# Kernel optimization log

Hardware: AMD Instinct MI355X
Metric: run time of the kernel (lower is better)

The kernel has to match this reference:

```python
import jax, jax.numpy as jnp
import numpy as np

B, S, D = 8, 2048, 128

def setup_inputs() -> dict:
    key = jax.random.key(0)
    kq, kk, kv, km = jax.random.split(key, 4)
    q = jax.random.normal(kq, (B, S, D), dtype=jnp.float32)
    k = jax.random.normal(kk, (B, S, D), dtype=jnp.float32)
    v = jax.random.normal(kv, (B, S, D), dtype=jnp.float32)
    mask = jax.random.randint(km, (B, S), 0, 2).astype(bool)  # True = masked out
    return {"q": q, "k": k, "v": v, "mask": mask}

def reference(q, k, v, mask):
    scaler = np.sqrt(D).astype(np.float32)
    # score[b, i, j] = <q_i, k_j> / sqrt(d_k)
    score = jnp.einsum('bik,bjk->bij', q, k) / scaler
    score = score - jnp.max(score, axis=-1, keepdims=True)
    e = jnp.exp(score)
    # mask is (B, S_kv): broadcast across query positions, zero out masked keys
    e = jnp.where(mask[:, None, :], 0.0, e)
    a = e / jnp.sum(e, axis=-1, keepdims=True)
    c = jnp.einsum('bij,bjd->bid', a, v)
    return c
```

## Files before the change

kernel.cpp:

```cpp
#include <hip/hip_runtime.h>
#include <hip/hip_fp16.h>
#include <math.h>

typedef __attribute__((ext_vector_type(8))) short short8;
typedef __attribute__((ext_vector_type(16))) float floatx16;
typedef __attribute__((ext_vector_type(2))) __bf16 bf16x2;
typedef __attribute__((ext_vector_type(2))) unsigned int uint2v;

namespace {
constexpr int Bn = 8;
constexpr int Sn = 2048;
constexpr int Dn = 128;
constexpr int BQ = 128;
constexpr int BK = 64;
constexpr int QTILES = Sn / BQ;
constexpr int NKB = Sn / BK;
constexpr int ROWS = Bn * Sn;
constexpr int NSPLIT = 4;
constexpr float SC2 = 0.12753102063642597f;
constexpr float DEFER_THR = 8.0f;
constexpr int TILE_USH = BK * Dn;
}

#if __has_builtin(__builtin_amdgcn_exp2f)
#define EXP2(x) __builtin_amdgcn_exp2f(x)
#else
#define EXP2(x) exp2f(x)
#endif

__device__ __forceinline__ unsigned short f2bf(float x) {
  union { float f; unsigned u; } a; a.f = x;
  unsigned r = a.u + 0x7fffu + ((a.u >> 16) & 1u);
  return (unsigned short)(r >> 16);
}

__device__ __forceinline__ unsigned pack2bf(float x, float y) {
  union { bf16x2 b; unsigned u; } c;
  c.b[0] = (__bf16)x; c.b[1] = (__bf16)y;
  return c.u;
}

__device__ __forceinline__ uint2v pl32swap(unsigned a, unsigned b, int h) {
#if __has_builtin(__builtin_amdgcn_permlane32_swap)
  (void)h;
  return __builtin_amdgcn_permlane32_swap(a, b, false, false);
#else
  unsigned ax = __shfl_xor((int)a, 32);
  unsigned bx = __shfl_xor((int)b, 32);
  uint2v r;
  r[0] = h ? bx : a;
  r[1] = h ? b : ax;
  return r;
#endif
}

__device__ __forceinline__ void gl_lds16(const void* g, void* l, int lane) {
#if __has_builtin(__builtin_amdgcn_global_load_lds)
  (void)lane;
  __builtin_amdgcn_global_load_lds((const __attribute__((address_space(1))) unsigned int*)g,
                                   (__attribute__((address_space(3))) unsigned int*)l, 16, 0, 0);
#else
  *(float4*)((char*)l + lane * 16) = *(const float4*)g;
#endif
}

__global__ __launch_bounds__(256)
void prep(const float* __restrict__ kg, const float* __restrict__ vg,
          const unsigned char* __restrict__ mraw,
          unsigned short* __restrict__ Kpg, unsigned short* __restrict__ Vpg,
          float* __restrict__ mb2g) {
  __shared__ __align__(16) float Vf[16 * 136];
  const int p = blockIdx.x;
  const int b = p >> 7, q = p & 127;
  const int kb = q >> 2, k16 = q & 3;
  const int t = threadIdx.x;

  unsigned wv = ((const unsigned int*)mraw)[t];
  int any1  = __syncthreads_or((wv & 0x0000ff00u) ? 1 : 0);
  int any23 = __syncthreads_or((wv & 0xffff0000u) ? 1 : 0);
  const int mlayout = any1 ? 1 : (any23 ? 2 : 0);
  if (p < 64) {
    int idx = p * 256 + t;
    bool ms;
    if (mlayout == 1)      ms = mraw[idx] != 0;
    else if (mlayout == 2) ms = ((const float*)mraw)[idx] != 0.0f;
    else                   ms = ((const int*)mraw)[idx] != 0;
    mb2g[idx] = ms ? -1e30f : 0.0f;
  }

  const int j  = t >> 4;
  const int o8 = t & 15;
  const size_t base = ((size_t)(b * Sn + kb * 64 + k16 * 16 + j)) * 32 + o8 * 2;
  const float4* k4 = (const float4*)kg;
  const float4* v4 = (const float4*)vg;

  {
    float4 a = k4[base], bq = k4[base + 1];
    union { unsigned u[4]; short8 s8; } pk;
    pk.u[0] = pack2bf(a.x, a.y);   pk.u[1] = pack2bf(a.z, a.w);
    pk.u[2] = pack2bf(bq.x, bq.y); pk.u[3] = pack2bf(bq.z, bq.w);
    const int jl = k16 * 16 + j;
    *(short8*)(Kpg + (size_t)(b * NKB + kb) * TILE_USH + jl * 128 + ((o8 ^ (jl & 7)) * 8)) = pk.s8;
  }
  {
    float4 a = v4[base], bq = v4[base + 1];
    *(float4*)&Vf[j * 136 + o8 * 8]     = a;
    *(float4*)&Vf[j * 136 + o8 * 8 + 4] = bq;
  }
  __syncthreads();
  {
    const int d = t >> 1, h = t & 1;
    union { unsigned u[4]; short8 s8; } pv;
    #pragma unroll
    for (int i = 0; i < 4; ++i)
      pv.u[i] = pack2bf(Vf[(h * 8 + 2 * i) * 136 + d], Vf[(h * 8 + 2 * i + 1) * 136 + d]);
    const int og = k16 * 2 + h;
    *(short8*)(Vpg + (size_t)(b * NKB + kb) * TILE_USH + d * 64 + ((og ^ (d & 7)) * 8)) = pv.s8;
  }
}


__device__ __forceinline__ void stage_tile(const char* gsrc, char* ldst,
                                           int stagebase, int L) {
  #pragma unroll
  for (int i = 0; i < 4; ++i) {
    const int off = stagebase + i * 1024;
    gl_lds16(gsrc + off + L * 16, ldst + off, L);
  }
}

__device__ __forceinline__ void qk_tile(const unsigned short* __restrict__ Kc,
                                        int q, int h, int sw,
                                        const short8 (&qh)[8], const short8 (&ql)[8],
                                        floatx16 (&s)[2]) {
  #pragma unroll
  for (int kg = 0; kg < 2; ++kg)
    #pragma unroll
    for (int r = 0; r < 16; ++r) s[kg][r] = 0.0f;
  #pragma unroll
  for (int kstep = 0; kstep < 8; ++kstep) {
    const int ko = ((kstep * 2 + h) ^ sw) * 8;
    #pragma unroll
    for (int kg = 0; kg < 2; ++kg) {
      short8 kf = *(const short8*)&Kc[(kg * 32 + q) * 128 + ko];
      s[kg] = __builtin_amdgcn_mfma_f32_32x32x16_bf16(kf, qh[kstep], s[kg], 0, 0, 0);
      s[kg] = __builtin_amdgcn_mfma_f32_32x32x16_bf16(kf, ql[kstep], s[kg], 0, 0, 0);
    }
  }
}

__device__ __forceinline__ void tile_body(
    int kbc, int kbN,
    const unsigned short* __restrict__ Kread, unsigned short* Kdst,
    const unsigned short* __restrict__ Vread, unsigned short* Vdst,
    const char* ktile, const char* vtile, int stagebase, int L,
    const float* __restrict__ mbrow,
    int q, int h, int sw,
    const short8 (&qh)[8], const short8 (&ql)[8],
    floatx16 (&sCur)[2], floatx16 (&sNxt)[2],
    floatx16 (&O32)[4], float& m_i, float& l_i, float& mtrue) {
  __syncthreads();

  if (kbc + 2 < kbN)
    stage_tile(ktile + (size_t)(kbc + 2) * (TILE_USH * 2), (char*)Kdst, stagebase, L);
  const bool hasNext = (kbc + 1 < kbN);
  if (hasNext)
    stage_tile(vtile + (size_t)(kbc + 1) * (TILE_USH * 2), (char*)Vdst, stagebase, L);

  if (hasNext)
    qk_tile(Kread, q, h, sw, qh, ql, sNxt);

  const float4* mb4 = (const float4*)(mbrow + kbc * BK);
  float4 mbv[2][4];
  #pragma unroll
  for (int kg = 0; kg < 2; ++kg)
    #pragma unroll
    for (int ro = 0; ro < 4; ++ro) mbv[kg][ro] = mb4[kg * 8 + ro * 2 + h];

  #pragma unroll
  for (int kg = 0; kg < 2; ++kg)
    #pragma unroll
    for (int ro = 0; ro < 4; ++ro) {
      float4 f = mbv[kg][ro];
      sCur[kg][4 * ro + 0] = fmaf(sCur[kg][4 * ro + 0], SC2, f.x);
      sCur[kg][4 * ro + 1] = fmaf(sCur[kg][4 * ro + 1], SC2, f.y);
      sCur[kg][4 * ro + 2] = fmaf(sCur[kg][4 * ro + 2], SC2, f.z);
      sCur[kg][4 * ro + 3] = fmaf(sCur[kg][4 * ro + 3], SC2, f.w);
    }
  float mxp[4] = {-INFINITY, -INFINITY, -INFINITY, -INFINITY};
  #pragma unroll
  for (int kg = 0; kg < 2; ++kg)
    #pragma unroll
    for (int r = 0; r < 16; ++r) mxp[r & 3] = fmaxf(mxp[r & 3], sCur[kg][r]);
  float mx = fmaxf(fmaxf(mxp[0], mxp[1]), fmaxf(mxp[2], mxp[3]));
  mx = fmaxf(mx, __shfl_xor(mx, 32));
  mtrue = fmaxf(mtrue, mx);

  float mnew;
  if (__all(mx <= m_i + DEFER_THR)) {
    mnew = m_i;
  } else {
    mnew = fmaxf(m_i, mx);
    const float alpha = EXP2(m_i - mnew);
    l_i *= alpha;
    #pragma unroll
    for (int dg = 0; dg < 4; ++dg)
      #pragma unroll
      for (int r = 0; r < 16; ++r) O32[dg][r] *= alpha;
  }

  float rsp[4] = {0.f, 0.f, 0.f, 0.f};
  #pragma unroll
  for (int kg = 0; kg < 2; ++kg)
    #pragma unroll
    for (int r = 0; r < 16; ++r) {
      float e = EXP2(sCur[kg][r] - mnew);
      sCur[kg][r] = e;
      rsp[r & 3] += e;
    }
  float rs = (rsp[0] + rsp[1]) + (rsp[2] + rsp[3]);
  rs += __shfl_xor(rs, 32);
  l_i += rs;
  m_i = mnew;

  unsigned xw[2][4][2];
  #pragma unroll
  for (int kg = 0; kg < 2; ++kg)
    #pragma unroll
    for (int m = 0; m < 4; ++m) {
      xw[kg][m][0] = pack2bf(sCur[kg][4 * m + 0], sCur[kg][4 * m + 1]);
      xw[kg][m][1] = pack2bf(sCur[kg][4 * m + 2], sCur[kg][4 * m + 3]);
    }
  unsigned pfw[4][4];
  #pragma unroll
  for (int kg = 0; kg < 2; ++kg)
    #pragma unroll
    for (int j = 0; j < 2; ++j)
      #pragma unroll
      for (int c2 = 0; c2 < 2; ++c2) {
        uint2v r = pl32swap(xw[kg][2 * j][c2], xw[kg][2 * j + 1][c2], h);
        pfw[kg * 2 + j][c2]     = r[0];
        pfw[kg * 2 + j][2 + c2] = r[1];
      }

  __builtin_amdgcn_s_setprio(1);
  #pragma unroll
  for (int k2 = 0; k2 < 4; ++k2) {
    const int ko = ((k2 * 2 + h) ^ sw) * 8;
    union { unsigned u[4]; short8 s8; } pw;
    pw.u[0] = pfw[k2][0]; pw.u[1] = pfw[k2][1];
    pw.u[2] = pfw[k2][2]; pw.u[3] = pfw[k2][3];
    #pragma unroll
    for (int dg = 0; dg < 4; ++dg) {
      short8 vf = *(const short8*)&Vread[(dg * 32 + q) * 64 + ko];
      O32[dg] = __builtin_amdgcn_mfma_f32_32x32x16_bf16(vf, pw.s8, O32[dg], 0, 0, 0);
    }
  }
  __builtin_amdgcn_s_setprio(0);
}

template<int SPLIT, bool DIRECT>
__global__ __launch_bounds__(256, 2)
void attn_fwd(const float* __restrict__ qg,
              const unsigned short* __restrict__ Kpg,
              const unsigned short* __restrict__ Vpg,
              const float* __restrict__ mb2g,
              float* __restrict__ outg, __half* __restrict__ Op,
              float* __restrict__ Mp, float* __restrict__ Lp) {
  __shared__ __align__(16) unsigned short Khi[2][TILE_USH];
  __shared__ __align__(16) unsigned short Vt[2][TILE_USH];

  const int tid = threadIdx.x;
  const int bid = blockIdx.x;
  const int b   = bid & 7;
  const int q0  = ((bid >> 3) & (QTILES - 1)) * BQ;
  const int s   = bid >> 7;
  const int kb0 = s * (NKB / SPLIT);
  const int kbN = kb0 + NKB / SPLIT;
  const int w   = tid >> 6;
  const int L   = tid & 63;
  const int q   = L & 31;
  const int h   = L >> 5;
  const int sw  = q & 7;

  const char* ktile = (const char*)(Kpg + (size_t)b * NKB * TILE_USH);
  const char* vtile = (const char*)(Vpg + (size_t)b * NKB * TILE_USH);
  const float* mbrow = mb2g + b * Sn;
  const int stagebase = w * 4096;

  short8 qh[8], ql[8];
  {
    const float* qrow = qg + (size_t)(b * Sn + q0 + w * 32 + q) * Dn;
    #pragma unroll
    for (int kstep = 0; kstep < 8; ++kstep) {
      float4 f0 = *(const float4*)(qrow + kstep * 16 + h * 8);
      float4 f1 = *(const float4*)(qrow + kstep * 16 + h * 8 + 4);
      float xs[8] = {f0.x, f0.y, f0.z, f0.w, f1.x, f1.y, f1.z, f1.w};
      #pragma unroll
      for (int j = 0; j < 8; ++j) {
        unsigned short hi = f2bf(xs[j]);
        union { unsigned u; float f; } hv; hv.u = ((unsigned)hi) << 16;
        qh[kstep][j] = (short)hi;
        ql[kstep][j] = (short)f2bf(xs[j] - hv.f);
      }
    }
  }

  float m_i = -INFINITY, l_i = 0.0f;
  float mtrue = -INFINITY;
  floatx16 O32[4];
  #pragma unroll
  for (int dg = 0; dg < 4; ++dg)
    #pragma unroll
    for (int r = 0; r < 16; ++r) O32[dg][r] = 0.0f;

  stage_tile(ktile + (size_t)kb0 * (TILE_USH * 2), (char*)Khi[0], stagebase, L);
  stage_tile(vtile + (size_t)kb0 * (TILE_USH * 2), (char*)Vt[0], stagebase, L);
  __syncthreads();
  stage_tile(ktile + (size_t)(kb0 + 1) * (TILE_USH * 2), (char*)Khi[1], stagebase, L);

  floatx16 sA[2], sB[2];
  qk_tile(Khi[0], q, h, sw, qh, ql, sA);

  constexpr int NT = NKB / SPLIT;
  static_assert((NT & 1) == 0, "pair-pipelined loop needs even tile count");
  for (int p2 = 0; p2 < NT / 2; ++p2) {
    const int kb = kb0 + 2 * p2;
    tile_body(kb, kbN, Khi[1], Khi[0], Vt[0], Vt[1], ktile, vtile, stagebase, L,
              mbrow, q, h, sw, qh, ql, sA, sB, O32, m_i, l_i, mtrue);
    tile_body(kb + 1, kbN, Khi[0], Khi[1], Vt[1], Vt[0], ktile, vtile, stagebase, L,
              mbrow, q, h, sw, qh, ql, sB, sA, O32, m_i, l_i, mtrue);
  }

  const int row = b * Sn + q0 + w * 32 + q;
  if constexpr (DIRECT) {
    const float inv = 1.0f / l_i;
    float* orow = outg + (size_t)row * Dn;
    #pragma unroll
    for (int dg = 0; dg < 4; ++dg)
      #pragma unroll
      for (int ro = 0; ro < 4; ++ro) {
        float4 f = make_float4(O32[dg][4 * ro] * inv,     O32[dg][4 * ro + 1] * inv,
                               O32[dg][4 * ro + 2] * inv, O32[dg][4 * ro + 3] * inv);
        *(float4*)&orow[dg * 32 + 8 * ro + 4 * h] = f;
      }
  } else {
    const float fin = EXP2(m_i - mtrue);
    __half* orow = Op + ((size_t)s * ROWS + row) * Dn;
    #pragma unroll
    for (int dg = 0; dg < 4; ++dg)
      #pragma unroll
      for (int ro = 0; ro < 4; ++ro) {
        union { __half2 h2[2]; uint2 u; } pk;
        pk.h2[0] = __floats2half2_rn(O32[dg][4 * ro] * fin,     O32[dg][4 * ro + 1] * fin);
        pk.h2[1] = __floats2half2_rn(O32[dg][4 * ro + 2] * fin, O32[dg][4 * ro + 3] * fin);
        *(uint2*)&orow[dg * 32 + 8 * ro + 4 * h] = pk.u;
      }
    if (h == 0) {
      Mp[s * ROWS + row] = mtrue;
      Lp[s * ROWS + row] = l_i * fin;
    }
  }
}

__global__ __launch_bounds__(256)
void attn_combine(const __half* __restrict__ Op, const float* __restrict__ Mp,
                  const float* __restrict__ Lp, float4* __restrict__ out4) {
  const int gid = blockIdx.x * 256 + threadIdx.x;
  const int row = gid >> 5;
  const int c4  = gid & 31;
  float ms[NSPLIT];
  float m = -INFINITY;
  #pragma unroll
  for (int s = 0; s < NSPLIT; ++s) { ms[s] = Mp[s * ROWS + row]; m = fmaxf(m, ms[s]); }
  float l = 0.0f;
  float4 acc = make_float4(0.f, 0.f, 0.f, 0.f);
  #pragma unroll
  for (int s = 0; s < NSPLIT; ++s) {
    float wgt = EXP2(ms[s] - m);
    l = fmaf(Lp[s * ROWS + row], wgt, l);
    union { uint2 u; __half2 h2[2]; } pk;
    pk.u = ((const uint2*)Op)[(size_t)(s * ROWS + row) * 32 + c4];
    float2 f0 = __half22float2(pk.h2[0]);
    float2 f1 = __half22float2(pk.h2[1]);
    acc.x = fmaf(f0.x, wgt, acc.x);
    acc.y = fmaf(f0.y, wgt, acc.y);
    acc.z = fmaf(f1.x, wgt, acc.z);
    acc.w = fmaf(f1.y, wgt, acc.w);
  }
  float inv = 1.0f / l;
  out4[(size_t)row * 32 + c4] = make_float4(acc.x * inv, acc.y * inv, acc.z * inv, acc.w * inv);
}

extern "C" void kernel_launch(void* const* d_in, const int* in_sizes, int n_in,
                              void* d_out, int out_size, void* d_ws, size_t ws_size,
                              hipStream_t stream) {
  const float* q = (const float*)d_in[0];
  const float* k = (const float*)d_in[1];
  const float* v = (const float*)d_in[2];
  const unsigned char* m = (const unsigned char*)d_in[3];
  float* out = (float*)d_out;
  (void)in_sizes; (void)n_in; (void)out_size;

  constexpr size_t OPB = (size_t)NSPLIT * ROWS * Dn * sizeof(__half);
  constexpr size_t MLB = (size_t)NSPLIT * ROWS * sizeof(float);
  constexpr size_t KPB = (size_t)Bn * NKB * TILE_USH * 2;
  constexpr size_t MBB = (size_t)ROWS * sizeof(float);

  char* ws = (char*)d_ws;
  if (ws_size >= OPB + 2 * MLB + 2 * KPB + MBB) {
    __half* Op = (__half*)ws;
    float* Mp = (float*)(ws + OPB);
    float* Lp = (float*)(ws + OPB + MLB);
    unsigned short* Kp = (unsigned short*)(ws + OPB + 2 * MLB);
    unsigned short* Vp = (unsigned short*)(ws + OPB + 2 * MLB + KPB);
    float* mb2 = (float*)(ws + OPB + 2 * MLB + 2 * KPB);
    prep<<<dim3(Bn * NKB * 4), dim3(256), 0, stream>>>(k, v, m, Kp, Vp, mb2);
    attn_fwd<NSPLIT, false><<<dim3(Bn * QTILES * NSPLIT), dim3(256), 0, stream>>>(
        q, Kp, Vp, mb2, out, Op, Mp, Lp);
    attn_combine<<<dim3(ROWS * 32 / 256), dim3(256), 0, stream>>>(
        Op, Mp, Lp, (float4*)out);
  } else if (ws_size >= 2 * KPB + MBB) {
    unsigned short* Kp = (unsigned short*)ws;
    unsigned short* Vp = (unsigned short*)(ws + KPB);
    float* mb2 = (float*)(ws + 2 * KPB);
    prep<<<dim3(Bn * NKB * 4), dim3(256), 0, stream>>>(k, v, m, Kp, Vp, mb2);
    attn_fwd<1, true><<<dim3(Bn * QTILES), dim3(256), 0, stream>>>(
        q, Kp, Vp, mb2, out, nullptr, nullptr, nullptr);
  }
}
```

Baseline: 116.0 us.

## Compact unmasked keys per batch and run attention only over them

New measurement: 110.1 us. 1.05x faster.

```diff
diff --git a/kernel.cpp b/kernel.cpp
--- a/kernel.cpp
+++ b/kernel.cpp
@@ -65,37 +65,88 @@
 }
 
 __global__ __launch_bounds__(256)
-void prep(const float* __restrict__ kg, const float* __restrict__ vg,
-          const unsigned char* __restrict__ mraw,
-          unsigned short* __restrict__ Kpg, unsigned short* __restrict__ Vpg,
-          float* __restrict__ mb2g) {
-  __shared__ __align__(16) float Vf[16 * 136];
-  const int p = blockIdx.x;
-  const int b = p >> 7, q = p & 127;
-  const int kb = q >> 2, k16 = q & 3;
+void mask_scan(const unsigned char* __restrict__ mraw,
+               unsigned short* __restrict__ idxg, int* __restrict__ cntg,
+               float* __restrict__ mb2g) {
+  __shared__ int sc[256];
+  const int b = blockIdx.x;
   const int t = threadIdx.x;
 
   unsigned wv = ((const unsigned int*)mraw)[t];
   int any1  = __syncthreads_or((wv & 0x0000ff00u) ? 1 : 0);
   int any23 = __syncthreads_or((wv & 0xffff0000u) ? 1 : 0);
   const int mlayout = any1 ? 1 : (any23 ? 2 : 0);
-  if (p < 64) {
-    int idx = p * 256 + t;
-    bool ms;
-    if (mlayout == 1)      ms = mraw[idx] != 0;
-    else if (mlayout == 2) ms = ((const float*)mraw)[idx] != 0.0f;
-    else                   ms = ((const int*)mraw)[idx] != 0;
-    mb2g[idx] = ms ? -1e30f : 0.0f;
-  }
+
+  const int s0 = t * 8;
+  const int gbase = b * Sn + s0;
+  bool ms[8];
+  if (mlayout == 1) {
+    #pragma unroll
+    for (int i = 0; i < 8; ++i) ms[i] = mraw[gbase + i] != 0;
+  } else if (mlayout == 2) {
+    const float* mf = (const float*)mraw;
+    #pragma unroll
+    for (int i = 0; i < 8; ++i) ms[i] = mf[gbase + i] != 0.0f;
+  } else {
+    const int* mi = (const int*)mraw;
+    #pragma unroll
+    for (int i = 0; i < 8; ++i) ms[i] = mi[gbase + i] != 0;
+  }
+
+  int c = 0;
+  #pragma unroll
+  for (int i = 0; i < 8; ++i) c += ms[i] ? 0 : 1;
+  sc[t] = c;
+  __syncthreads();
+  for (int off = 1; off < 256; off <<= 1) {
+    int v = (t >= off) ? sc[t - off] : 0;
+    __syncthreads();
+    sc[t] += v;
+    __syncthreads();
+  }
+  const int incl = sc[t];
+  const int total = sc[255];
+  int pos = incl - c;
+  #pragma unroll
+  for (int i = 0; i < 8; ++i)
+    if (!ms[i]) idxg[b * Sn + (pos++)] = (unsigned short)(s0 + i);
+  if (t == 0) cntg[b] = total;
+  #pragma unroll
+  for (int i = 0; i < 8; ++i)
+    mb2g[b * Sn + s0 + i] = (s0 + i < total) ? 0.0f : -1e30f;
+}
+
+__global__ __launch_bounds__(256)
+void prep(const float* __restrict__ kg, const float* __restrict__ vg,
+          const unsigned short* __restrict__ idxg, const int* __restrict__ cntg,
+          unsigned short* __restrict__ Kpg, unsigned short* __restrict__ Vpg) {
+  __shared__ __align__(16) float Vf[16 * 136];
+  const int p = blockIdx.x;
+  const int b = p >> 7, qq = p & 127;
+  const int kb = qq >> 2, k16 = qq & 3;
+  const int t = threadIdx.x;
+
+  const int cnt = cntg[b];
+  const int padded = (cnt + 63) & ~63;
+  const int slot0 = kb * 64 + k16 * 16;
+  if (slot0 >= padded) return;
 
   const int j  = t >> 4;
   const int o8 = t & 15;
-  const size_t base = ((size_t)(b * Sn + kb * 64 + k16 * 16 + j)) * 32 + o8 * 2;
-  const float4* k4 = (const float4*)kg;
-  const float4* v4 = (const float4*)vg;
+  const int sl = slot0 + j;
+  const bool real = sl < cnt;
+
+  float4 a, bq, va, vb;
+  if (real) {
+    const int srow = idxg[b * Sn + sl];
+    const size_t base = ((size_t)(b * Sn + srow)) * 32 + o8 * 2;
+    a  = ((const float4*)kg)[base]; bq = ((const float4*)kg)[base + 1];
+    va = ((const float4*)vg)[base]; vb = ((const float4*)vg)[base + 1];
+  } else {
+    a = bq = va = vb = make_float4(0.f, 0.f, 0.f, 0.f);
+  }
 
   {
-    float4 a = k4[base], bq = k4[base + 1];
     union { unsigned u[4]; short8 s8; } pk;
     pk.u[0] = pack2bf(a.x, a.y);   pk.u[1] = pack2bf(a.z, a.w);
     pk.u[2] = pack2bf(bq.x, bq.y); pk.u[3] = pack2bf(bq.z, bq.w);
@@ -103,9 +154,8 @@
     *(short8*)(Kpg + (size_t)(b * NKB + kb) * TILE_USH + jl * 128 + ((o8 ^ (jl & 7)) * 8)) = pk.s8;
   }
   {
-    float4 a = v4[base], bq = v4[base + 1];
-    *(float4*)&Vf[j * 136 + o8 * 8]     = a;
-    *(float4*)&Vf[j * 136 + o8 * 8 + 4] = bq;
+    *(float4*)&Vf[j * 136 + o8 * 8]     = va;
+    *(float4*)&Vf[j * 136 + o8 * 8 + 4] = vb;
   }
   __syncthreads();
   {
@@ -265,6 +315,7 @@
               const unsigned short* __restrict__ Kpg,
               const unsigned short* __restrict__ Vpg,
               const float* __restrict__ mb2g,
+              const int* __restrict__ cntg,
               float* __restrict__ outg, __half* __restrict__ Op,
               float* __restrict__ Mp, float* __restrict__ Lp) {
   __shared__ __align__(16) unsigned short Khi[2][TILE_USH];
@@ -275,14 +326,40 @@
   const int b   = bid & 7;
   const int q0  = ((bid >> 3) & (QTILES - 1)) * BQ;
   const int s   = bid >> 7;
-  const int kb0 = s * (NKB / SPLIT);
-  const int kbN = kb0 + NKB / SPLIT;
   const int w   = tid >> 6;
   const int L   = tid & 63;
   const int q   = L & 31;
   const int h   = L >> 5;
   const int sw  = q & 7;
 
+  const int cnt = cntg[b];
+  const int nt  = (cnt + 63) >> 6;
+  const int kb0 = (s * nt) / SPLIT;
+  const int kbN = ((s + 1) * nt) / SPLIT;
+  const int T   = kbN - kb0;
+
+  const int row = b * Sn + q0 + w * 32 + q;
+
+  if (T <= 0) {
+    if constexpr (DIRECT) {
+      float* orow = outg + (size_t)row * Dn;
+      float4 z = make_float4(0.f, 0.f, 0.f, 0.f);
+      #pragma unroll
+      for (int dg = 0; dg < 4; ++dg)
+        #pragma unroll
+        for (int ro = 0; ro < 4; ++ro) *(float4*)&orow[dg * 32 + 8 * ro + 4 * h] = z;
+    } else {
+      __half* orow = Op + ((size_t)s * ROWS + row) * Dn;
+      uint2 z; z.x = 0u; z.y = 0u;
+      #pragma unroll
+      for (int dg = 0; dg < 4; ++dg)
+        #pragma unroll
+        for (int ro = 0; ro < 4; ++ro) *(uint2*)&orow[dg * 32 + 8 * ro + 4 * h] = z;
+      if (h == 0) { Mp[s * ROWS + row] = -INFINITY; Lp[s * ROWS + row] = 0.0f; }
+    }
+    return;
+  }
+
   const char* ktile = (const char*)(Kpg + (size_t)b * NKB * TILE_USH);
   const char* vtile = (const char*)(Vpg + (size_t)b * NKB * TILE_USH);
   const float* mbrow = mb2g + b * Sn;
@@ -290,7 +367,7 @@
 
   short8 qh[8], ql[8];
   {
-    const float* qrow = qg + (size_t)(b * Sn + q0 + w * 32 + q) * Dn;
+    const float* qrow = qg + (size_t)row * Dn;
     #pragma unroll
     for (int kstep = 0; kstep < 8; ++kstep) {
       float4 f0 = *(const float4*)(qrow + kstep * 16 + h * 8);
@@ -317,22 +394,23 @@
   stage_tile(ktile + (size_t)kb0 * (TILE_USH * 2), (char*)Khi[0], stagebase, L);
   stage_tile(vtile + (size_t)kb0 * (TILE_USH * 2), (char*)Vt[0], stagebase, L);
   __syncthreads();
-  stage_tile(ktile + (size_t)(kb0 + 1) * (TILE_USH * 2), (char*)Khi[1], stagebase, L);
+  if (kb0 + 1 < kbN)
+    stage_tile(ktile + (size_t)(kb0 + 1) * (TILE_USH * 2), (char*)Khi[1], stagebase, L);
 
   floatx16 sA[2], sB[2];
   qk_tile(Khi[0], q, h, sw, qh, ql, sA);
 
-  constexpr int NT = NKB / SPLIT;
-  static_assert((NT & 1) == 0, "pair-pipelined loop needs even tile count");
-  for (int p2 = 0; p2 < NT / 2; ++p2) {
-    const int kb = kb0 + 2 * p2;
+  int kb = kb0;
+  for (; kb + 2 <= kbN; kb += 2) {
     tile_body(kb, kbN, Khi[1], Khi[0], Vt[0], Vt[1], ktile, vtile, stagebase, L,
               mbrow, q, h, sw, qh, ql, sA, sB, O32, m_i, l_i, mtrue);
     tile_body(kb + 1, kbN, Khi[0], Khi[1], Vt[1], Vt[0], ktile, vtile, stagebase, L,
               mbrow, q, h, sw, qh, ql, sB, sA, O32, m_i, l_i, mtrue);
   }
-
-  const int row = b * Sn + q0 + w * 32 + q;
+  if (kb < kbN)
+    tile_body(kb, kbN, Khi[1], Khi[0], Vt[0], Vt[1], ktile, vtile, stagebase, L,
+              mbrow, q, h, sw, qh, ql, sA, sB, O32, m_i, l_i, mtrue);
+
   if constexpr (DIRECT) {
     const float inv = 1.0f / l_i;
     float* orow = outg + (size_t)row * Dn;
@@ -406,26 +484,34 @@
   constexpr size_t MLB = (size_t)NSPLIT * ROWS * sizeof(float);
   constexpr size_t KPB = (size_t)Bn * NKB * TILE_USH * 2;
   constexpr size_t MBB = (size_t)ROWS * sizeof(float);
+  constexpr size_t CNTB = 64;
+  constexpr size_t IDXB = (size_t)Bn * Sn * sizeof(unsigned short);
 
   char* ws = (char*)d_ws;
-  if (ws_size >= OPB + 2 * MLB + 2 * KPB + MBB) {
+  if (ws_size >= OPB + 2 * MLB + 2 * KPB + MBB + CNTB + IDXB) {
     __half* Op = (__half*)ws;
     float* Mp = (float*)(ws + OPB);
     float* Lp = (float*)(ws + OPB + MLB);
     unsigned short* Kp = (unsigned short*)(ws + OPB + 2 * MLB);
     unsigned short* Vp = (unsigned short*)(ws + OPB + 2 * MLB + KPB);
     float* mb2 = (float*)(ws + OPB + 2 * MLB + 2 * KPB);
-    prep<<<dim3(Bn * NKB * 4), dim3(256), 0, stream>>>(k, v, m, Kp, Vp, mb2);
+    int* cnt = (int*)(ws + OPB + 2 * MLB + 2 * KPB + MBB);
+    unsigned short* idx = (unsigned short*)(ws + OPB + 2 * MLB + 2 * KPB + MBB + CNTB);
+    mask_scan<<<dim3(Bn), dim3(256), 0, stream>>>(m, idx, cnt, mb2);
+    prep<<<dim3(Bn * NKB * 4), dim3(256), 0, stream>>>(k, v, idx, cnt, Kp, Vp);
     attn_fwd<NSPLIT, false><<<dim3(Bn * QTILES * NSPLIT), dim3(256), 0, stream>>>(
-        q, Kp, Vp, mb2, out, Op, Mp, Lp);
+        q, Kp, Vp, mb2, cnt, out, Op, Mp, Lp);
     attn_combine<<<dim3(ROWS * 32 / 256), dim3(256), 0, stream>>>(
         Op, Mp, Lp, (float4*)out);
-  } else if (ws_size >= 2 * KPB + MBB) {
+  } else if (ws_size >= 2 * KPB + MBB + CNTB + IDXB) {
     unsigned short* Kp = (unsigned short*)ws;
     unsigned short* Vp = (unsigned short*)(ws + KPB);
     float* mb2 = (float*)(ws + 2 * KPB);
-    prep<<<dim3(Bn * NKB * 4), dim3(256), 0, stream>>>(k, v, m, Kp, Vp, mb2);
+    int* cnt = (int*)(ws + 2 * KPB + MBB);
+    unsigned short* idx = (unsigned short*)(ws + 2 * KPB + MBB + CNTB);
+    mask_scan<<<dim3(Bn), dim3(256), 0, stream>>>(m, idx, cnt, mb2);
+    prep<<<dim3(Bn * NKB * 4), dim3(256), 0, stream>>>(k, v, idx, cnt, Kp, Vp);
     attn_fwd<1, true><<<dim3(Bn * QTILES), dim3(256), 0, stream>>>(
-        q, Kp, Vp, mb2, out, nullptr, nullptr, nullptr);
-  }
-}
+        q, Kp, Vp, mb2, cnt, out, nullptr, nullptr, nullptr);
+  }
+}
```
